# Performance work log

Hardware: AMD Instinct MI355X
Metric: run time of the kernel (lower is better)

Reference implementation:

```python
import jax, jax.numpy as jnp
import numpy as np

HIDDEN = 2048
NUM_HEADS = 16
HEAD_DIM = HIDDEN // NUM_HEADS
REWARD_DIM = 1
B, S = 2, 2048


def setup_inputs() -> dict:
    key = jax.random.key(0)
    ks = jax.random.split(key, 16)
    std = 0.02
    inp = {
        "query": jax.random.normal(ks[0], (B, S, HIDDEN), jnp.float32),
        "key": jax.random.normal(ks[1], (B, S, HIDDEN), jnp.float32),
        "value": jax.random.normal(ks[2], (B, S, HIDDEN), jnp.float32),
        "rewards": jax.random.normal(ks[3], (B, S, REWARD_DIM), jnp.float32),
        "attention_mask": jnp.ones((B, S), dtype=bool),
        # linear params stored as (in, out); apply as x @ W + b
        "Wq": jax.random.normal(ks[4], (HIDDEN, HIDDEN), jnp.float32) * std,
        "bq": jnp.zeros((HIDDEN,), jnp.float32),
        "Wk": jax.random.normal(ks[5], (HIDDEN, HIDDEN), jnp.float32) * std,
        "bk": jnp.zeros((HIDDEN,), jnp.float32),
        "Wv": jax.random.normal(ks[6], (HIDDEN, HIDDEN), jnp.float32) * std,
        "bv": jnp.zeros((HIDDEN,), jnp.float32),
        "Wo": jax.random.normal(ks[7], (HIDDEN, HIDDEN), jnp.float32) * std,
        "bo": jnp.zeros((HIDDEN,), jnp.float32),
        "Wr": jax.random.normal(ks[8], (REWARD_DIM, HIDDEN), jnp.float32) * std,
        "br": jnp.zeros((HIDDEN,), jnp.float32),
        "Wa": jax.random.normal(ks[9], (HIDDEN, NUM_HEADS), jnp.float32) * std,
        "ba": jnp.zeros((NUM_HEADS,), jnp.float32),
    }
    return inp


def reference(query, key, value, rewards, attention_mask,
              Wq, bq, Wk, bk, Wv, bv, Wo, bo, Wr, br, Wa, ba):
    b, s, h = query.shape
    nh, hd = NUM_HEADS, HEAD_DIM
    scale = hd ** -0.5

    q = (query @ Wq + bq).reshape(b, s, nh, hd).transpose(0, 2, 1, 3)  # [b,nh,s,hd]
    k = (key @ Wk + bk).reshape(b, s, nh, hd).transpose(0, 2, 1, 3)
    v = (value @ Wv + bv).reshape(b, s, nh, hd).transpose(0, 2, 1, 3)

    # reward-conditioned per-(batch, head, query) additive bias
    reward_features = rewards @ Wr + br           # [b,s,hidden]
    reward_bias = reward_features @ Wa + ba        # [b,s,nh]
    reward_bias = reward_bias.transpose(0, 2, 1)[..., None]  # [b,nh,s,1]

    scores = jnp.einsum("bhqd,bhkd->bhqk", q, k) * scale + reward_bias
    scores = jnp.where(attention_mask[:, None, None, :], scores, -1e9)

    attention_weights = jax.nn.softmax(scores, axis=-1)        # [b,nh,s,s]
    attended = jnp.einsum("bhqk,bhkd->bqhd", attention_weights, v)
    attended = attended.reshape(b, s, h)
    output = attended @ Wo + bo
    return output, attention_weights.mean(axis=1)
```

## Files before the change

kernel.cpp:

```cpp
#include <hip/hip_runtime.h>

typedef unsigned short u16;
typedef __attribute__((ext_vector_type(8))) short bf16x8;
typedef __attribute__((ext_vector_type(8))) unsigned short u16x8;
typedef __attribute__((ext_vector_type(4))) unsigned short u16x4;
typedef __attribute__((ext_vector_type(4))) float f32x4;

#define MFMA16(a, b, c) __builtin_amdgcn_mfma_f32_16x16x32_bf16((a), (b), (c), 0, 0, 0)
#define SCALE 0.08838834764831845f

__device__ __forceinline__ u16 f2bf(float f) {
    union { float f; unsigned int u; } x; x.f = f;
    unsigned int lsb = (x.u >> 16) & 1u;
    return (u16)((x.u + 0x7FFFu + lsb) >> 16);
}

__global__ __launch_bounds__(256) void transpose_k(const float* __restrict__ W, u16* __restrict__ WT) {
    __shared__ u16 tile[128][136];
    const int tid = threadIdx.x;
    const int k0 = blockIdx.y * 128, n0 = blockIdx.x * 128;
#pragma unroll
    for (int i = 0; i < 16; i++) {
        int idx = tid + i * 256;
        int r = idx >> 5, c4 = (idx & 31) * 4;
        f32x4 v = *(const f32x4*)(W + (size_t)(k0 + r) * 2048 + n0 + c4);
#pragma unroll
        for (int j = 0; j < 4; j++) tile[c4 + j][r] = f2bf(v[j]);
    }
    __syncthreads();
#pragma unroll
    for (int i = 0; i < 8; i++) {
        int idx = tid + i * 256;
        int r = idx >> 4, c = (idx & 15) * 8;
        *(u16x8*)(WT + (size_t)(n0 + r) * 2048 + k0 + c) = *(const u16x8*)&tile[r][c];
    }
}

__global__ __launch_bounds__(256) void vt_k(const u16* __restrict__ V, u16* __restrict__ VT) {
    const int bh = blockIdx.y, s0 = blockIdx.x * 128;
    const u16* src = V + ((size_t)bh * 2048 + s0) * 128;
    u16* dst = VT + (size_t)bh * 262144 + s0;
    const int bi = threadIdx.x >> 4;
    const int bj = threadIdx.x & 15;
    u16x8 v[8];
#pragma unroll
    for (int r = 0; r < 8; r++) v[r] = *(const u16x8*)(src + (size_t)(bi * 8 + r) * 128 + bj * 8);
#pragma unroll
    for (int c = 0; c < 8; c++) {
        u16x8 t;
#pragma unroll
        for (int r = 0; r < 8; r++) t[r] = v[r][c];
        *(u16x8*)(dst + (size_t)(bj * 8 + c) * 2048 + bi * 8) = t;
    }
}

template <int MODE>
__global__ __launch_bounds__(256) void gemm_k(const void* __restrict__ Av, const u16* __restrict__ WT,
                                              const float* __restrict__ bias, void* __restrict__ Cv) {
    __shared__ u16 As[128][40];
    __shared__ u16 Bs[128][40];
    const int tid = threadIdx.x;
    const int wave = tid >> 6, lane = tid & 63;
    const int wm = wave >> 1, wn = wave & 1;
    const int quad = lane >> 4, l15 = lane & 15;
    const int m0 = blockIdx.y * 128, n0 = blockIdx.x * 128;

    f32x4 acc[4][4];
#pragma unroll
    for (int a = 0; a < 4; a++)
#pragma unroll
        for (int b = 0; b < 4; b++) acc[a][b] = (f32x4){0.f, 0.f, 0.f, 0.f};

    for (int k0 = 0; k0 < 2048; k0 += 32) {
        __syncthreads();
        if (MODE == 0) {
            const float* A = (const float*)Av;
#pragma unroll
            for (int i = 0; i < 4; i++) {
                int idx = tid + i * 256;
                int r = idx >> 3, c4 = (idx & 7) * 4;
                f32x4 v = *(const f32x4*)(A + (size_t)(m0 + r) * 2048 + k0 + c4);
                u16x4 p;
#pragma unroll
                for (int j = 0; j < 4; j++) p[j] = f2bf(v[j]);
                *(u16x4*)&As[r][c4] = p;
            }
        } else {
            const u16* A = (const u16*)Av;
#pragma unroll
            for (int i = 0; i < 2; i++) {
                int idx = tid + i * 256;
                int r = idx >> 2, sg = (idx & 3) * 8;
                int m = m0 + r, k = k0 + sg;
                size_t aoff = ((size_t)((m >> 11) * 16 + (k >> 7)) * 2048 + (m & 2047)) * 128 + (k & 127);
                *(u16x8*)&As[r][sg] = *(const u16x8*)(A + aoff);
            }
        }
#pragma unroll
        for (int i = 0; i < 2; i++) {
            int idx = tid + i * 256;
            int r = idx >> 2, sg = (idx & 3) * 8;
            *(u16x8*)&Bs[r][sg] = *(const u16x8*)(WT + (size_t)(n0 + r) * 2048 + (k0 + sg));
        }
        __syncthreads();
        bf16x8 af[4], bfv[4];
#pragma unroll
        for (int mt = 0; mt < 4; mt++) af[mt] = *(const bf16x8*)&As[wm * 64 + mt * 16 + l15][quad * 8];
#pragma unroll
        for (int nt = 0; nt < 4; nt++) bfv[nt] = *(const bf16x8*)&Bs[wn * 64 + nt * 16 + l15][quad * 8];
#pragma unroll
        for (int mt = 0; mt < 4; mt++)
#pragma unroll
            for (int nt = 0; nt < 4; nt++) acc[mt][nt] = MFMA16(af[mt], bfv[nt], acc[mt][nt]);
    }

    float bv[4];
#pragma unroll
    for (int nt = 0; nt < 4; nt++) bv[nt] = bias[n0 + wn * 64 + nt * 16 + l15];

#pragma unroll
    for (int mt = 0; mt < 4; mt++) {
        int rb = wm * 64 + mt * 16 + quad * 4;
#pragma unroll
        for (int nt = 0; nt < 4; nt++) {
            int col = n0 + wn * 64 + nt * 16 + l15;
#pragma unroll
            for (int reg = 0; reg < 4; reg++) {
                int grow = m0 + rb + reg;
                float val = acc[mt][nt][reg] + bv[nt];
                if (MODE == 0) {
                    size_t coff = ((size_t)((grow >> 11) * 16 + (col >> 7)) * 2048 + (grow & 2047)) * 128 + (col & 127);
                    ((u16*)Cv)[coff] = f2bf(val);
                } else {
                    ((float*)Cv)[(size_t)grow * 2048 + col] = val;
                }
            }
        }
    }
}

__global__ __launch_bounds__(256) void flash2_k(const u16* __restrict__ Q, const u16* __restrict__ K,
                                                const u16* __restrict__ VT, u16* __restrict__ att,
                                                float* __restrict__ ML) {
    __shared__ u16 sh[64 * 144 + 128 * 80];
    u16* Ks = sh;
    u16* Vs = sh + 64 * 144;

    const int tid = threadIdx.x;
    const int wave = tid >> 6, lane = tid & 63;
    const int quad = lane >> 4, l15 = lane & 15;
    const int bh = blockIdx.x & 31;
    const int q0 = (blockIdx.x >> 5) * 128;
    const size_t ho = (size_t)bh * 262144;
    const int qw = wave * 32;

    bf16x8 bq[2][4];
#pragma unroll
    for (int nt = 0; nt < 2; nt++)
#pragma unroll
        for (int df = 0; df < 4; df++)
            bq[nt][df] = *(const bf16x8*)(Q + ho + (size_t)(q0 + qw + nt * 16 + l15) * 128 + df * 32 + quad * 8);

    f32x4 acc[8][2];
#pragma unroll
    for (int a = 0; a < 8; a++)
#pragma unroll
        for (int b = 0; b < 2; b++) acc[a][b] = (f32x4){0.f, 0.f, 0.f, 0.f};
    float m_[2] = {-1e30f, -1e30f}, l_[2] = {0.f, 0.f};

    for (int kt = 0; kt < 32; kt++) {
        __syncthreads();
#pragma unroll
        for (int i = 0; i < 4; i++) {
            int idx = tid + i * 256, r = idx >> 4, c = (idx & 15) * 8;
            *(u16x8*)&Ks[r * 144 + c] = *(const u16x8*)(K + ho + (size_t)(kt * 64 + r) * 128 + c);
        }
#pragma unroll
        for (int i = 0; i < 4; i++) {
            int idx = tid + i * 256, d = idx >> 3, u = idx & 7;
            *(u16x8*)&Vs[d * 80 + u * 8] = *(const u16x8*)(VT + ho + (size_t)d * 2048 + kt * 64 + u * 8);
        }
        __syncthreads();

        f32x4 st[4][2];
#pragma unroll
        for (int t = 0; t < 4; t++)
#pragma unroll
            for (int nt = 0; nt < 2; nt++) st[t][nt] = (f32x4){0.f, 0.f, 0.f, 0.f};
#pragma unroll
        for (int df = 0; df < 4; df++) {
#pragma unroll
            for (int t = 0; t < 4; t++) {
                bf16x8 ak = *(const bf16x8*)&Ks[(t * 16 + l15) * 144 + df * 32 + quad * 8];
                st[t][0] = MFMA16(ak, bq[0][df], st[t][0]);
                st[t][1] = MFMA16(ak, bq[1][df], st[t][1]);
            }
        }

        float corr[2], colsum[2];
        int pw[4][2][2];
#pragma unroll
        for (int nt = 0; nt < 2; nt++) {
            float tm = -1e30f;
#pragma unroll
            for (int t = 0; t < 4; t++)
#pragma unroll
                for (int reg = 0; reg < 4; reg++) tm = fmaxf(tm, st[t][nt][reg]);
            tm = fmaxf(tm, __shfl_xor(tm, 16));
            tm = fmaxf(tm, __shfl_xor(tm, 32));
            tm *= SCALE;
            float mn = fmaxf(m_[nt], tm);
            corr[nt] = __expf(m_[nt] - mn);
            m_[nt] = mn;
            float cs = 0.f;
#pragma unroll
            for (int t = 0; t < 4; t++) {
                float p0 = __expf(st[t][nt][0] * SCALE - mn);
                float p1 = __expf(st[t][nt][1] * SCALE - mn);
                float p2 = __expf(st[t][nt][2] * SCALE - mn);
                float p3 = __expf(st[t][nt][3] * SCALE - mn);
                cs += (p0 + p1) + (p2 + p3);
                pw[t][nt][0] = (int)f2bf(p0) | ((int)f2bf(p1) << 16);
                pw[t][nt][1] = (int)f2bf(p2) | ((int)f2bf(p3) << 16);
            }
            cs += __shfl_xor(cs, 16);
            cs += __shfl_xor(cs, 32);
            l_[nt] = l_[nt] * corr[nt] + cs;
        }
#pragma unroll
        for (int mt = 0; mt < 8; mt++)
#pragma unroll
            for (int nt = 0; nt < 2; nt++) {
                acc[mt][nt][0] *= corr[nt]; acc[mt][nt][1] *= corr[nt];
                acc[mt][nt][2] *= corr[nt]; acc[mt][nt][3] *= corr[nt];
            }

        const int s0l = 32 * (quad & 1) + l15, s1l = s0l + 16;
        const bool hi = quad >= 2;
#pragma unroll
        for (int kf = 0; kf < 2; kf++) {
            bf16x8 bp[2];
#pragma unroll
            for (int nt = 0; nt < 2; nt++) {
                int tA = kf * 2, tB = kf * 2 + 1;
                int a0A = __shfl(pw[tA][nt][0], s0l), a0B = __shfl(pw[tB][nt][0], s0l);
                int a1A = __shfl(pw[tA][nt][1], s0l), a1B = __shfl(pw[tB][nt][1], s0l);
                int a2A = __shfl(pw[tA][nt][0], s1l), a2B = __shfl(pw[tB][nt][0], s1l);
                int a3A = __shfl(pw[tA][nt][1], s1l), a3B = __shfl(pw[tB][nt][1], s1l);
                union { int w[4]; bf16x8 v; } u;
                u.w[0] = hi ? a0B : a0A;
                u.w[1] = hi ? a1B : a1A;
                u.w[2] = hi ? a2B : a2A;
                u.w[3] = hi ? a3B : a3A;
                bp[nt] = u.v;
            }
#pragma unroll
            for (int mt = 0; mt < 8; mt++) {
                bf16x8 av = *(const bf16x8*)&Vs[(mt * 16 + l15) * 80 + kf * 32 + quad * 8];
                acc[mt][0] = MFMA16(av, bp[0], acc[mt][0]);
                acc[mt][1] = MFMA16(av, bp[1], acc[mt][1]);
            }
        }
    }

    if (quad == 0) {
#pragma unroll
        for (int nt = 0; nt < 2; nt++)
            ML[(size_t)bh * 2048 + q0 + qw + nt * 16 + l15] = m_[nt] + __logf(l_[nt]);
    }

    __syncthreads();
    u16* Ot = Ks;
    float inv0 = 1.f / l_[0], inv1 = 1.f / l_[1];
#pragma unroll
    for (int mt = 0; mt < 8; mt++)
#pragma unroll
        for (int reg = 0; reg < 4; reg++) {
            int d = mt * 16 + quad * 4 + reg;
            Ot[(qw + l15) * 136 + d] = f2bf(acc[mt][0][reg] * inv0);
            Ot[(qw + 16 + l15) * 136 + d] = f2bf(acc[mt][1][reg] * inv1);
        }
    __syncthreads();
#pragma unroll
    for (int i = 0; i < 8; i++) {
        int idx = tid + i * 256, r = idx >> 4, c = (idx & 15) * 8;
        *(u16x8*)(att + ho + (size_t)(q0 + r) * 128 + c) = *(const u16x8*)&Ot[r * 136 + c];
    }
}

__global__ __launch_bounds__(256) void meanw_k(const u16* __restrict__ Q, const u16* __restrict__ K,
                                               const float* __restrict__ ML, float* __restrict__ W2) {
    __shared__ u16 Ks[128][136];
    __shared__ float ml_s[64];
    const int tid = threadIdx.x;
    const int wave = tid >> 6, lane = tid & 63;
    const int wm = wave >> 1, wn = wave & 1;
    const int quad = lane >> 4, l15 = lane & 15;
    const int k0 = blockIdx.x * 128, q0 = blockIdx.y * 64, bb = blockIdx.z;

    f32x4 macc[2][4];
#pragma unroll
    for (int a = 0; a < 2; a++)
#pragma unroll
        for (int b = 0; b < 4; b++) macc[a][b] = (f32x4){0.f, 0.f, 0.f, 0.f};

    for (int h = 0; h < 16; h++) {
        __syncthreads();
        const size_t ho = (size_t)(bb * 16 + h) * 262144;
        const u16* kb = K + ho + (size_t)k0 * 128;
#pragma unroll
        for (int i = 0; i < 8; i++) {
            int idx = tid + i * 256;
            int rr = idx >> 4, c = (idx & 15) * 8;
            *(u16x8*)&Ks[rr][c] = *(const u16x8*)(kb + (size_t)rr * 128 + c);
        }
        if (tid < 64) ml_s[tid] = ML[(size_t)(bb * 16 + h) * 2048 + q0 + tid];
        __syncthreads();
        const u16* qb = Q + ho + (size_t)q0 * 128;
        bf16x8 aq[2][4];
#pragma unroll
        for (int mt = 0; mt < 2; mt++)
#pragma unroll
            for (int ks = 0; ks < 4; ks++)
                aq[mt][ks] = *(const bf16x8*)(qb + (size_t)(wm * 32 + mt * 16 + l15) * 128 + ks * 32 + quad * 8);
#pragma unroll
        for (int mt = 0; mt < 2; mt++) {
            int rb = wm * 32 + mt * 16 + quad * 4;
#pragma unroll
            for (int nt = 0; nt < 4; nt++) {
                f32x4 s4 = (f32x4){0.f, 0.f, 0.f, 0.f};
#pragma unroll
                for (int ks = 0; ks < 4; ks++) {
                    bf16x8 bk = *(const bf16x8*)&Ks[wn * 64 + nt * 16 + l15][ks * 32 + quad * 8];
                    s4 = MFMA16(aq[mt][ks], bk, s4);
                }
#pragma unroll
                for (int reg = 0; reg < 4; reg++)
                    macc[mt][nt][reg] += __expf(s4[reg] * SCALE - ml_s[rb + reg]);
            }
        }
    }
#pragma unroll
    for (int mt = 0; mt < 2; mt++) {
        int rb = wm * 32 + mt * 16 + quad * 4;
#pragma unroll
        for (int nt = 0; nt < 4; nt++) {
            int col = k0 + wn * 64 + nt * 16 + l15;
#pragma unroll
            for (int reg = 0; reg < 4; reg++) {
                int row = q0 + rb + reg;
                W2[((size_t)bb * 2048 + row) * 2048 + col] = macc[mt][nt][reg] * 0.0625f;
            }
        }
    }
}

extern "C" void kernel_launch(void* const* d_in, const int* in_sizes, int n_in,
                              void* d_out, int out_size, void* d_ws, size_t ws_size,
                              hipStream_t stream) {
    (void)in_sizes; (void)n_in; (void)out_size; (void)ws_size;
    const float* query = (const float*)d_in[0];
    const float* key   = (const float*)d_in[1];
    const float* value = (const float*)d_in[2];
    const float* Wq = (const float*)d_in[5];
    const float* bq = (const float*)d_in[6];
    const float* Wk = (const float*)d_in[7];
    const float* bk = (const float*)d_in[8];
    const float* Wv = (const float*)d_in[9];
    const float* bv = (const float*)d_in[10];
    const float* Wo = (const float*)d_in[11];
    const float* bo = (const float*)d_in[12];

    float* out1 = (float*)d_out;
    float* out2 = out1 + (size_t)2 * 2048 * 2048;

    u16* qt  = (u16*)d_ws;
    u16* ktw = qt  + (size_t)8388608;
    u16* WoT = ktw + (size_t)8388608;
    float* MLb = (float*)(WoT + (size_t)4194304);
    u16* Wt1 = (u16*)out1;
    u16* vtw = Wt1 + (size_t)4194304;
    u16* att = (u16*)out2;
    u16* vtT = att + (size_t)8388608;

    dim3 tg(16, 16);
    dim3 gg(16, 32);

    transpose_k<<<tg, 256, 0, stream>>>(Wq, Wt1);
    gemm_k<0><<<gg, 256, 0, stream>>>(query, Wt1, bq, qt);
    transpose_k<<<tg, 256, 0, stream>>>(Wk, Wt1);
    gemm_k<0><<<gg, 256, 0, stream>>>(key,   Wt1, bk, ktw);
    transpose_k<<<tg, 256, 0, stream>>>(Wv, Wt1);
    gemm_k<0><<<gg, 256, 0, stream>>>(value, Wt1, bv, vtw);

    vt_k<<<dim3(16, 32), 256, 0, stream>>>(vtw, vtT);
    flash2_k<<<512, 256, 0, stream>>>(qt, ktw, vtT, att, MLb);

    transpose_k<<<tg, 256, 0, stream>>>(Wo, WoT);
    gemm_k<1><<<gg, 256, 0, stream>>>(att, WoT, bo, out1);

    meanw_k<<<dim3(16, 32, 2), 256, 0, stream>>>(qt, ktw, MLb, out2);
}
```

Measured before the change: 716.3 us.

## Pre-convert inputs to bf16, async LDS double-buffered GEMM, row-major head layout, exp2

Adds a standalone fp32->bf16 conversion kernel so the projection GEMMs read bf16 activations, and rewrites the GEMM main loop to double-buffer shared memory via global_load_lds direct-to-LDS copies. Q/K/V/attention outputs now stay in plain row-major [b*s, hidden] layout with coalesced stores through an LDS staging tile, and the attention kernels index heads by column offset. The softmax scale and log2(e) are folded into Q during projection so flash and mean-weight kernels use exp2 directly. Adds extra conversion launches and traffic, and relies on unpadded LDS tiles that may cause bank conflicts.

```diff
diff --git a/kernel.cpp b/kernel.cpp
--- a/kernel.cpp
+++ b/kernel.cpp
@@ -7,13 +7,31 @@
 typedef __attribute__((ext_vector_type(4))) float f32x4;
 
 #define MFMA16(a, b, c) __builtin_amdgcn_mfma_f32_16x16x32_bf16((a), (b), (c), 0, 0, 0)
-#define SCALE 0.08838834764831845f
+#define QSCALE (0.08838834764831845f * 1.4426950408889634f)
+
+#define GLDS(l, g) __builtin_amdgcn_global_load_lds((const __attribute__((address_space(1))) void*)(g), \
+                                                    (__attribute__((address_space(3))) void*)(l), 16, 0, 0)
 
 __device__ __forceinline__ u16 f2bf(float f) {
     union { float f; unsigned int u; } x; x.f = f;
     unsigned int lsb = (x.u >> 16) & 1u;
     return (u16)((x.u + 0x7FFFu + lsb) >> 16);
 }
+__device__ __forceinline__ float exp2v(float x) {
+    return __builtin_amdgcn_exp2f(x);
+}
+
+__global__ __launch_bounds__(256) void cvt_k(const float* __restrict__ in, u16* __restrict__ out) {
+    const size_t stride = (size_t)gridDim.x * 2048;
+    for (size_t i = ((size_t)blockIdx.x * 256 + threadIdx.x) * 8; i < 8388608; i += stride) {
+        f32x4 a = *(const f32x4*)(in + i);
+        f32x4 b = *(const f32x4*)(in + i + 4);
+        u16x8 p;
+#pragma unroll
+        for (int j = 0; j < 4; j++) { p[j] = f2bf(a[j]); p[4 + j] = f2bf(b[j]); }
+        *(u16x8*)(out + i) = p;
+    }
+}
 
 __global__ __launch_bounds__(256) void transpose_k(const float* __restrict__ W, u16* __restrict__ WT) {
     __shared__ u16 tile[128][136];
@@ -38,13 +56,14 @@
 
 __global__ __launch_bounds__(256) void vt_k(const u16* __restrict__ V, u16* __restrict__ VT) {
     const int bh = blockIdx.y, s0 = blockIdx.x * 128;
-    const u16* src = V + ((size_t)bh * 2048 + s0) * 128;
+    const int b = bh >> 4, h = bh & 15;
+    const u16* src = V + (size_t)(b * 2048 + s0) * 2048 + h * 128;
     u16* dst = VT + (size_t)bh * 262144 + s0;
     const int bi = threadIdx.x >> 4;
     const int bj = threadIdx.x & 15;
     u16x8 v[8];
 #pragma unroll
-    for (int r = 0; r < 8; r++) v[r] = *(const u16x8*)(src + (size_t)(bi * 8 + r) * 128 + bj * 8);
+    for (int r = 0; r < 8; r++) v[r] = *(const u16x8*)(src + (size_t)(bi * 8 + r) * 2048 + bj * 8);
 #pragma unroll
     for (int c = 0; c < 8; c++) {
         u16x8 t;
@@ -54,87 +73,103 @@
     }
 }
 
-template <int MODE>
-__global__ __launch_bounds__(256) void gemm_k(const void* __restrict__ Av, const u16* __restrict__ WT,
-                                              const float* __restrict__ bias, void* __restrict__ Cv) {
-    __shared__ u16 As[128][40];
-    __shared__ u16 Bs[128][40];
+template <int F32OUT>
+__global__ __launch_bounds__(256) void gemm_k(const u16* __restrict__ A, const u16* __restrict__ WT,
+                                              const float* __restrict__ bias, void* __restrict__ Cv,
+                                              float scale) {
+    __shared__ __align__(16) u16 sh[17408];
     const int tid = threadIdx.x;
     const int wave = tid >> 6, lane = tid & 63;
     const int wm = wave >> 1, wn = wave & 1;
     const int quad = lane >> 4, l15 = lane & 15;
     const int m0 = blockIdx.y * 128, n0 = blockIdx.x * 128;
 
+    const u16* aPtr[2]; const u16* bPtr[2]; int sOff[2];
+#pragma unroll
+    for (int i = 0; i < 2; i++) {
+        int ck = i * 4 + wave;
+        int r = ck * 16 + (lane >> 2);
+        int ce = (lane & 3) * 8;
+        aPtr[i] = A + (size_t)(m0 + r) * 2048 + ce;
+        bPtr[i] = WT + (size_t)(n0 + r) * 2048 + ce;
+        sOff[i] = ck * 512;
+    }
     f32x4 acc[4][4];
 #pragma unroll
     for (int a = 0; a < 4; a++)
 #pragma unroll
         for (int b = 0; b < 4; b++) acc[a][b] = (f32x4){0.f, 0.f, 0.f, 0.f};
 
+#pragma unroll
+    for (int i = 0; i < 2; i++) {
+        GLDS(sh + sOff[i], aPtr[i]);
+        GLDS(sh + 4096 + sOff[i], bPtr[i]);
+        aPtr[i] += 32; bPtr[i] += 32;
+    }
+    __syncthreads();
+
+    int cur = 0;
     for (int k0 = 0; k0 < 2048; k0 += 32) {
-        __syncthreads();
-        if (MODE == 0) {
-            const float* A = (const float*)Av;
-#pragma unroll
-            for (int i = 0; i < 4; i++) {
-                int idx = tid + i * 256;
-                int r = idx >> 3, c4 = (idx & 7) * 4;
-                f32x4 v = *(const f32x4*)(A + (size_t)(m0 + r) * 2048 + k0 + c4);
-                u16x4 p;
-#pragma unroll
-                for (int j = 0; j < 4; j++) p[j] = f2bf(v[j]);
-                *(u16x4*)&As[r][c4] = p;
-            }
-        } else {
-            const u16* A = (const u16*)Av;
+        if (k0 < 2016) {
+            u16* db = sh + (cur ^ 1) * 8192;
 #pragma unroll
             for (int i = 0; i < 2; i++) {
-                int idx = tid + i * 256;
-                int r = idx >> 2, sg = (idx & 3) * 8;
-                int m = m0 + r, k = k0 + sg;
-                size_t aoff = ((size_t)((m >> 11) * 16 + (k >> 7)) * 2048 + (m & 2047)) * 128 + (k & 127);
-                *(u16x8*)&As[r][sg] = *(const u16x8*)(A + aoff);
-            }
-        }
-#pragma unroll
-        for (int i = 0; i < 2; i++) {
-            int idx = tid + i * 256;
-            int r = idx >> 2, sg = (idx & 3) * 8;
-            *(u16x8*)&Bs[r][sg] = *(const u16x8*)(WT + (size_t)(n0 + r) * 2048 + (k0 + sg));
-        }
-        __syncthreads();
+                GLDS(db + sOff[i], aPtr[i]);
+                GLDS(db + 4096 + sOff[i], bPtr[i]);
+                aPtr[i] += 32; bPtr[i] += 32;
+            }
+        }
+        const u16* As = sh + cur * 8192;
+        const u16* Bs = As + 4096;
         bf16x8 af[4], bfv[4];
 #pragma unroll
-        for (int mt = 0; mt < 4; mt++) af[mt] = *(const bf16x8*)&As[wm * 64 + mt * 16 + l15][quad * 8];
-#pragma unroll
-        for (int nt = 0; nt < 4; nt++) bfv[nt] = *(const bf16x8*)&Bs[wn * 64 + nt * 16 + l15][quad * 8];
+        for (int mt = 0; mt < 4; mt++) af[mt] = *(const bf16x8*)&As[(wm * 64 + mt * 16 + l15) * 32 + quad * 8];
+#pragma unroll
+        for (int nt = 0; nt < 4; nt++) bfv[nt] = *(const bf16x8*)&Bs[(wn * 64 + nt * 16 + l15) * 32 + quad * 8];
 #pragma unroll
         for (int mt = 0; mt < 4; mt++)
 #pragma unroll
             for (int nt = 0; nt < 4; nt++) acc[mt][nt] = MFMA16(af[mt], bfv[nt], acc[mt][nt]);
+        __syncthreads();
+        cur ^= 1;
     }
 
     float bv[4];
 #pragma unroll
     for (int nt = 0; nt < 4; nt++) bv[nt] = bias[n0 + wn * 64 + nt * 16 + l15];
 
-#pragma unroll
-    for (int mt = 0; mt < 4; mt++) {
-        int rb = wm * 64 + mt * 16 + quad * 4;
-#pragma unroll
-        for (int nt = 0; nt < 4; nt++) {
-            int col = n0 + wn * 64 + nt * 16 + l15;
-#pragma unroll
-            for (int reg = 0; reg < 4; reg++) {
-                int grow = m0 + rb + reg;
-                float val = acc[mt][nt][reg] + bv[nt];
-                if (MODE == 0) {
-                    size_t coff = ((size_t)((grow >> 11) * 16 + (col >> 7)) * 2048 + (grow & 2047)) * 128 + (col & 127);
-                    ((u16*)Cv)[coff] = f2bf(val);
-                } else {
-                    ((float*)Cv)[(size_t)grow * 2048 + col] = val;
-                }
-            }
+    if (F32OUT) {
+        float* C = (float*)Cv;
+#pragma unroll
+        for (int mt = 0; mt < 4; mt++) {
+            int rb = wm * 64 + mt * 16 + quad * 4;
+#pragma unroll
+            for (int nt = 0; nt < 4; nt++) {
+                int col = n0 + wn * 64 + nt * 16 + l15;
+#pragma unroll
+                for (int reg = 0; reg < 4; reg++)
+                    C[(size_t)(m0 + rb + reg) * 2048 + col] = acc[mt][nt][reg] + bv[nt];
+            }
+        }
+    } else {
+        u16* Ot = sh;
+#pragma unroll
+        for (int mt = 0; mt < 4; mt++) {
+            int rb = wm * 64 + mt * 16 + quad * 4;
+#pragma unroll
+            for (int nt = 0; nt < 4; nt++) {
+                int cl = wn * 64 + nt * 16 + l15;
+#pragma unroll
+                for (int reg = 0; reg < 4; reg++)
+                    Ot[(rb + reg) * 136 + cl] = f2bf((acc[mt][nt][reg] + bv[nt]) * scale);
+            }
+        }
+        __syncthreads();
+        u16* C = (u16*)Cv;
+#pragma unroll
+        for (int i = 0; i < 8; i++) {
+            int idx = tid + i * 256, r = idx >> 4, c = (idx & 15) * 8;
+            *(u16x8*)(C + (size_t)(m0 + r) * 2048 + n0 + c) = *(const u16x8*)&Ot[r * 136 + c];
         }
     }
 }
@@ -142,7 +177,7 @@
 __global__ __launch_bounds__(256) void flash2_k(const u16* __restrict__ Q, const u16* __restrict__ K,
                                                 const u16* __restrict__ VT, u16* __restrict__ att,
                                                 float* __restrict__ ML) {
-    __shared__ u16 sh[64 * 144 + 128 * 80];
+    __shared__ __align__(16) u16 sh[64 * 144 + 128 * 80];
     u16* Ks = sh;
     u16* Vs = sh + 64 * 144;
 
@@ -150,8 +185,9 @@
     const int wave = tid >> 6, lane = tid & 63;
     const int quad = lane >> 4, l15 = lane & 15;
     const int bh = blockIdx.x & 31;
+    const int bB = bh >> 4, h = bh & 15;
     const int q0 = (blockIdx.x >> 5) * 128;
-    const size_t ho = (size_t)bh * 262144;
+    const size_t vo = (size_t)bh * 262144;
     const int qw = wave * 32;
 
     bf16x8 bq[2][4];
@@ -159,7 +195,7 @@
     for (int nt = 0; nt < 2; nt++)
 #pragma unroll
         for (int df = 0; df < 4; df++)
-            bq[nt][df] = *(const bf16x8*)(Q + ho + (size_t)(q0 + qw + nt * 16 + l15) * 128 + df * 32 + quad * 8);
+            bq[nt][df] = *(const bf16x8*)(Q + (size_t)(bB * 2048 + q0 + qw + nt * 16 + l15) * 2048 + h * 128 + df * 32 + quad * 8);
 
     f32x4 acc[8][2];
 #pragma unroll
@@ -173,12 +209,12 @@
 #pragma unroll
         for (int i = 0; i < 4; i++) {
             int idx = tid + i * 256, r = idx >> 4, c = (idx & 15) * 8;
-            *(u16x8*)&Ks[r * 144 + c] = *(const u16x8*)(K + ho + (size_t)(kt * 64 + r) * 128 + c);
+            *(u16x8*)&Ks[r * 144 + c] = *(const u16x8*)(K + (size_t)(bB * 2048 + kt * 64 + r) * 2048 + h * 128 + c);
         }
 #pragma unroll
         for (int i = 0; i < 4; i++) {
             int idx = tid + i * 256, d = idx >> 3, u = idx & 7;
-            *(u16x8*)&Vs[d * 80 + u * 8] = *(const u16x8*)(VT + ho + (size_t)d * 2048 + kt * 64 + u * 8);
+            *(u16x8*)&Vs[d * 80 + u * 8] = *(const u16x8*)(VT + vo + (size_t)d * 2048 + kt * 64 + u * 8);
         }
         __syncthreads();
 
@@ -197,7 +233,7 @@
             }
         }
 
-        float corr[2], colsum[2];
+        float corr[2];
         int pw[4][2][2];
 #pragma unroll
         for (int nt = 0; nt < 2; nt++) {
@@ -208,17 +244,16 @@
                 for (int reg = 0; reg < 4; reg++) tm = fmaxf(tm, st[t][nt][reg]);
             tm = fmaxf(tm, __shfl_xor(tm, 16));
             tm = fmaxf(tm, __shfl_xor(tm, 32));
-            tm *= SCALE;
             float mn = fmaxf(m_[nt], tm);
-            corr[nt] = __expf(m_[nt] - mn);
+            corr[nt] = exp2v(m_[nt] - mn);
             m_[nt] = mn;
             float cs = 0.f;
 #pragma unroll
             for (int t = 0; t < 4; t++) {
-                float p0 = __expf(st[t][nt][0] * SCALE - mn);
-                float p1 = __expf(st[t][nt][1] * SCALE - mn);
-                float p2 = __expf(st[t][nt][2] * SCALE - mn);
-                float p3 = __expf(st[t][nt][3] * SCALE - mn);
+                float p0 = exp2v(st[t][nt][0] - mn);
+                float p1 = exp2v(st[t][nt][1] - mn);
+                float p2 = exp2v(st[t][nt][2] - mn);
+                float p3 = exp2v(st[t][nt][3] - mn);
                 cs += (p0 + p1) + (p2 + p3);
                 pw[t][nt][0] = (int)f2bf(p0) | ((int)f2bf(p1) << 16);
                 pw[t][nt][1] = (int)f2bf(p2) | ((int)f2bf(p3) << 16);
@@ -266,7 +301,7 @@
     if (quad == 0) {
 #pragma unroll
         for (int nt = 0; nt < 2; nt++)
-            ML[(size_t)bh * 2048 + q0 + qw + nt * 16 + l15] = m_[nt] + __logf(l_[nt]);
+            ML[(size_t)bh * 2048 + q0 + qw + nt * 16 + l15] = m_[nt] + __log2f(l_[nt]);
     }
 
     __syncthreads();
@@ -284,13 +319,13 @@
 #pragma unroll
     for (int i = 0; i < 8; i++) {
         int idx = tid + i * 256, r = idx >> 4, c = (idx & 15) * 8;
-        *(u16x8*)(att + ho + (size_t)(q0 + r) * 128 + c) = *(const u16x8*)&Ot[r * 136 + c];
+        *(u16x8*)(att + (size_t)(bB * 2048 + q0 + r) * 2048 + h * 128 + c) = *(const u16x8*)&Ot[r * 136 + c];
     }
 }
 
 __global__ __launch_bounds__(256) void meanw_k(const u16* __restrict__ Q, const u16* __restrict__ K,
                                                const float* __restrict__ ML, float* __restrict__ W2) {
-    __shared__ u16 Ks[128][136];
+    __shared__ __align__(16) u16 Ks[128][136];
     __shared__ float ml_s[64];
     const int tid = threadIdx.x;
     const int wave = tid >> 6, lane = tid & 63;
@@ -306,23 +341,22 @@
 
     for (int h = 0; h < 16; h++) {
         __syncthreads();
-        const size_t ho = (size_t)(bb * 16 + h) * 262144;
-        const u16* kb = K + ho + (size_t)k0 * 128;
+        const u16* kb = K + (size_t)(bb * 2048 + k0) * 2048 + h * 128;
 #pragma unroll
         for (int i = 0; i < 8; i++) {
             int idx = tid + i * 256;
             int rr = idx >> 4, c = (idx & 15) * 8;
-            *(u16x8*)&Ks[rr][c] = *(const u16x8*)(kb + (size_t)rr * 128 + c);
+            *(u16x8*)&Ks[rr][c] = *(const u16x8*)(kb + (size_t)rr * 2048 + c);
         }
         if (tid < 64) ml_s[tid] = ML[(size_t)(bb * 16 + h) * 2048 + q0 + tid];
         __syncthreads();
-        const u16* qb = Q + ho + (size_t)q0 * 128;
+        const u16* qb = Q + (size_t)(bb * 2048 + q0) * 2048 + h * 128;
         bf16x8 aq[2][4];
 #pragma unroll
         for (int mt = 0; mt < 2; mt++)
 #pragma unroll
             for (int ks = 0; ks < 4; ks++)
-                aq[mt][ks] = *(const bf16x8*)(qb + (size_t)(wm * 32 + mt * 16 + l15) * 128 + ks * 32 + quad * 8);
+                aq[mt][ks] = *(const bf16x8*)(qb + (size_t)(wm * 32 + mt * 16 + l15) * 2048 + ks * 32 + quad * 8);
 #pragma unroll
         for (int mt = 0; mt < 2; mt++) {
             int rb = wm * 32 + mt * 16 + quad * 4;
@@ -336,7 +370,7 @@
                 }
 #pragma unroll
                 for (int reg = 0; reg < 4; reg++)
-                    macc[mt][nt][reg] += __expf(s4[reg] * SCALE - ml_s[rb + reg]);
+                    macc[mt][nt][reg] += exp2v(s4[reg] - ml_s[rb + reg]);
             }
         }
     }
@@ -375,29 +409,34 @@
     float* out2 = out1 + (size_t)2 * 2048 * 2048;
 
     u16* qt  = (u16*)d_ws;
-    u16* ktw = qt  + (size_t)8388608;
+    u16* ktw = qt + (size_t)8388608;
     u16* WoT = ktw + (size_t)8388608;
     float* MLb = (float*)(WoT + (size_t)4194304);
     u16* Wt1 = (u16*)out1;
-    u16* vtw = Wt1 + (size_t)4194304;
+    u16* qb  = Wt1 + (size_t)4194304;
     u16* att = (u16*)out2;
     u16* vtT = att + (size_t)8388608;
 
     dim3 tg(16, 16);
     dim3 gg(16, 32);
 
+    cvt_k<<<2048, 256, 0, stream>>>(query, qb);
     transpose_k<<<tg, 256, 0, stream>>>(Wq, Wt1);
-    gemm_k<0><<<gg, 256, 0, stream>>>(query, Wt1, bq, qt);
+    gemm_k<0><<<gg, 256, 0, stream>>>(qb, Wt1, bq, qt, (float)QSCALE);
+
+    cvt_k<<<2048, 256, 0, stream>>>(key, qb);
     transpose_k<<<tg, 256, 0, stream>>>(Wk, Wt1);
-    gemm_k<0><<<gg, 256, 0, stream>>>(key,   Wt1, bk, ktw);
+    gemm_k<0><<<gg, 256, 0, stream>>>(qb, Wt1, bk, ktw, 1.f);
+
+    cvt_k<<<2048, 256, 0, stream>>>(value, qb);
     transpose_k<<<tg, 256, 0, stream>>>(Wv, Wt1);
-    gemm_k<0><<<gg, 256, 0, stream>>>(value, Wt1, bv, vtw);
-
-    vt_k<<<dim3(16, 32), 256, 0, stream>>>(vtw, vtT);
+    gemm_k<0><<<gg, 256, 0, stream>>>(qb, Wt1, bv, att , 1.f);
+
+    vt_k<<<dim3(16, 32), 256, 0, stream>>>(att , vtT);
     flash2_k<<<512, 256, 0, stream>>>(qt, ktw, vtT, att, MLb);
 
     transpose_k<<<tg, 256, 0, stream>>>(Wo, WoT);
-    gemm_k<1><<<gg, 256, 0, stream>>>(att, WoT, bo, out1);
+    gemm_k<1><<<gg, 256, 0, stream>>>(att, WoT, bo, out1, 1.f);
 
     meanw_k<<<dim3(16, 32, 2), 256, 0, stream>>>(qt, ktw, MLb, out2);
 }
```

After: 693.9 us. -3.1%, faster.
